# Optimization experiments

Measured on AMD Instinct MI355X. Metric: run time of the kernel, lower is better.

Reference implementation:

```python
import jax, jax.numpy as jnp
import numpy as np

SWITCH_W = 30.0
TOL = 5
DECAY = 0.7
FP_PEN = 10.0
INV_PEN = 100.0
CLASS_W = jnp.array([1.0, 1.0, SWITCH_W, SWITCH_W], dtype=jnp.float32)


def setup_inputs() -> dict:
    key = jax.random.key(0)
    k1, k2, k3 = jax.random.split(key, 3)
    B, S, C = 512, 8192, 4
    logits = jax.random.normal(k1, (B, S, C), dtype=jnp.float32)
    labels = jax.random.randint(k2, (B, S), 0, 4, dtype=jnp.int32)
    # sprinkle ignore_index (-100) positions like real padded sequences
    drop = jax.random.uniform(k3, (B, S)) < 0.05
    labels = jnp.where(drop, jnp.int32(-100), labels)
    return {"logits": logits, "labels": labels}


def _mode_multiplier(labels, preds):
    """Sequential state machine over time; carry = (pred_mode, true_mode) per batch row."""
    B, S = labels.shape

    def step(carry, xs):
        pm, tm = carry
        lab, pred = xs  # [B] each
        valid = lab != -100
        # invalid transition penalty on predicted switches
        bad = ((pred == 2) & (pm == 0)) | ((pred == 3) & (pm == 1))
        pen = jnp.where(valid & bad, INV_PEN, 1.0)
        new_pm = jnp.where(valid, jnp.where((pred == 0) | (pred == 2), 0, 1), pm)
        # reward correct mode switches (true label agrees with pred switch)
        good = ((lab == 2) & (tm == 1) & (pred == 2)) | ((lab == 3) & (tm == 0) & (pred == 3))
        bonus = jnp.where(valid & good, 0.1, 1.0)
        new_tm = jnp.where(valid & ((lab == 0) | (lab == 2)), 0,
                           jnp.where(valid & ((lab == 1) | (lab == 3)), 1, tm))
        return (new_pm, new_tm), pen * bonus

    init = (jnp.zeros((B,), jnp.int32), jnp.zeros((B,), jnp.int32))
    _, mult = jax.lax.scan(step, init, (labels.T, preds.T))
    return mult.T  # [B, S]


def _nearest_dist(mask):
    """For each position, distance to nearest True in the same row; BIG if none."""
    B, S = mask.shape
    BIG = jnp.int32(S + TOL + 2)

    def f(c, m):
        c = jnp.where(m, jnp.int32(0), jnp.minimum(c + 1, BIG))
        return c, c

    init = jnp.full((B,), BIG, jnp.int32)
    _, fwd = jax.lax.scan(f, init, mask.T)
    _, bwd = jax.lax.scan(f, init, mask[:, ::-1].T)
    return jnp.minimum(fwd.T, bwd.T[:, ::-1])


def _loss(logits, labels):
    preds = jnp.argmax(logits, axis=-1).astype(jnp.int32)
    valid = labels != -100
    labs = jnp.where(valid, labels, 0)
    logp = jax.nn.log_softmax(logits, axis=-1)
    ce = -jnp.take_along_axis(logp, labs[..., None], axis=-1)[..., 0] * CLASS_W[labs]

    mult = _mode_multiplier(labels, preds)
    for c in (2, 3):
        true_m = labels == c
        pred_m = preds == c
        d_true = _nearest_dist(true_m)
        d_pred = _nearest_dist(pred_m)
        has_true = true_m.any(axis=1, keepdims=True)
        has_pred = pred_m.any(axis=1, keepdims=True)
        # multipliers at predicted-switch positions
        mp = jnp.where(
            pred_m,
            jnp.where(
                has_true,
                jnp.where(d_true == 0, 0.1,
                          jnp.where(d_true <= TOL, DECAY ** d_true.astype(jnp.float32), FP_PEN)),
                FP_PEN * 2.0),
            1.0)
        # multipliers at true-switch positions
        mt = jnp.where(
            true_m,
            jnp.where(has_pred, jnp.where(d_pred > TOL, 2.0, 1.0), 3.0),
            1.0)
        mult = mult * mp * mt

    vf = valid.astype(ce.dtype)
    total = (ce * mult * vf).sum()
    return total / jnp.maximum(vf.sum(), 1.0)


def reference(logits, labels):
    return _loss(logits, labels)
```

## Files before the change

kernel.cpp:

```cpp
#include <hip/hip_runtime.h>
#include <math.h>

#define BROWS 512
#define SLEN  8192
#define NT    1024
#define CHUNK (SLEN / NT)
#define NWRD  (SLEN / 32)
#define MWRD  (NWRD + 2)

__device__ __forceinline__ int win_dist(const unsigned int* __restrict__ M, int t) {
    int sI = t + 27;
    int w  = sI >> 5;
    int off = sI & 31;
    unsigned long long val =
        ((unsigned long long)M[w] | ((unsigned long long)M[w + 1] << 32)) >> off;
    unsigned int win = (unsigned int)val & 0x7FFu;
    if (win & 32u) return 0;
    unsigned int dn = win & 31u;
    unsigned int up = (win >> 6) & 31u;
    int d = 99;
    if (dn) d = 5 - (31 - __clz((int)dn));
    if (up) { int du = __ffs((int)up); if (du < d) d = du; }
    return d;
}

__device__ __forceinline__ float decay_pow(int d) {
    return (d == 1) ? 0.7f : (d == 2) ? 0.49f : (d == 3) ? 0.343f
         : (d == 4) ? 0.2401f : 0.16807f;
}

__global__ __launch_bounds__(NT, 8) void row_loss_kernel(
    const float* __restrict__ logits, const int* __restrict__ labels,
    double* __restrict__ psum, unsigned int* __restrict__ pcnt)
{
    __shared__ float         s_ce[SLEN];
    __shared__ unsigned char s_pk[SLEN];
    __shared__ unsigned int  s_m[4][MWRD];
    __shared__ unsigned int  s_wave[16];
    __shared__ unsigned int  s_wavex[16];
    __shared__ unsigned int  s_flags;
    __shared__ double        s_red[16];
    __shared__ int           s_redc[16];

    const int row  = blockIdx.x;
    const int tid  = threadIdx.x;
    const int lane = tid & 63;
    const int wid  = tid >> 6;

    if (tid < 8) s_m[tid >> 1][(tid & 1) ? (MWRD - 1) : 0] = 0u;
    if (tid == 0) s_flags = 0u;

    const float4* lg4 = (const float4*)(logits + (size_t)row * SLEN * 4);
    const int*    lb  = labels + (size_t)row * SLEN;

    int cnt = 0;
    #pragma unroll
    for (int kk = 0; kk < CHUNK; kk += 4) {
        float4 v[4]; int la[4];
        #pragma unroll
        for (int j = 0; j < 4; ++j) {
            int t = (kk + j) * NT + tid;
            v[j]  = lg4[t];
            la[j] = lb[t];
        }
        #pragma unroll
        for (int j = 0; j < 4; ++j) {
            int t = (kk + j) * NT + tid;
            float4 q = v[j];
            int lab  = la[j];
            float m01 = fmaxf(q.x, q.y), m23 = fmaxf(q.z, q.w);
            float best = fmaxf(m01, m23);
            int pred = (best == q.x) ? 0 : (best == q.y) ? 1 : (best == q.z) ? 2 : 3;
            bool valid = (lab != -100);
            cnt += valid ? 1 : 0;
            int l = valid ? (lab & 3) : 0;
            float se = __expf(q.x - best) + __expf(q.y - best) +
                       __expf(q.z - best) + __expf(q.w - best);
            float lse = best + __logf(se);
            float xl = (l == 0) ? q.x : (l == 1) ? q.y : (l == 2) ? q.z : q.w;
            float wc = (l >= 2) ? 30.0f : 1.0f;
            s_ce[t] = valid ? (lse - xl) * wc : 0.0f;
            s_pk[t] = (unsigned char)(pred | (l << 2) | (valid ? 16 : 0));
        }
    }
    __syncthreads();

    const int base = tid * CHUNK;
    const unsigned long long pkw = *(const unsigned long long*)(s_pk + base);
    unsigned int mt2 = 0, mp2 = 0, mt3 = 0, mp3 = 0;
    unsigned int summary = 0;
    #pragma unroll
    for (int i = 0; i < CHUNK; ++i) {
        unsigned int pk = (unsigned int)(pkw >> (8 * i)) & 31u;
        int pred = pk & 3, l = (pk >> 2) & 3;
        bool valid = (pk & 16) != 0;
        if (pred == 2) mp2 |= 1u << i;
        if (pred == 3) mp3 |= 1u << i;
        if (valid && l == 2) mt2 |= 1u << i;
        if (valid && l == 3) mt3 |= 1u << i;
        if (valid) summary = 4u | (unsigned)(pred & 1) | ((unsigned)(l & 1) << 1);
    }
    {
        int sh = (tid & 3) * 8;
        unsigned int w0 = mt2 << sh, w1 = mp2 << sh, w2 = mt3 << sh, w3 = mp3 << sh;
        w0 |= __shfl_xor(w0, 1); w0 |= __shfl_xor(w0, 2);
        w1 |= __shfl_xor(w1, 1); w1 |= __shfl_xor(w1, 2);
        w2 |= __shfl_xor(w2, 1); w2 |= __shfl_xor(w2, 2);
        w3 |= __shfl_xor(w3, 1); w3 |= __shfl_xor(w3, 2);
        if ((tid & 3) == 0) {
            int wi = 1 + (tid >> 2);
            s_m[0][wi] = w0; s_m[1][wi] = w1; s_m[2][wi] = w2; s_m[3][wi] = w3;
        }
    }
    {
        unsigned int fl = (mt2 ? 1u : 0u) | (mp2 ? 2u : 0u) |
                          (mt3 ? 4u : 0u) | (mp3 ? 8u : 0u);
        #pragma unroll
        for (int s = 32; s > 0; s >>= 1) fl |= __shfl_xor(fl, s);
        if (lane == 0 && fl) atomicOr(&s_flags, fl);
    }

    unsigned int inc = summary;
    #pragma unroll
    for (int st = 1; st < 64; st <<= 1) {
        unsigned int o = __shfl_up(inc, st);
        if (lane >= st && !(inc & 4u)) inc = o;
    }
    unsigned int exc = __shfl_up(inc, 1);
    if (lane == 0) exc = 0u;
    if (lane == 63) s_wave[wid] = inc;
    __syncthreads();
    if (wid == 0) {
        unsigned int wv = (lane < 16) ? s_wave[lane] : 0u;
        #pragma unroll
        for (int st = 1; st < 16; st <<= 1) {
            unsigned int o = __shfl_up(wv, st);
            if (lane >= st && !(wv & 4u)) wv = o;
        }
        unsigned int wex = __shfl_up(wv, 1);
        if (lane == 0) wex = 0u;
        if (lane < 16) s_wavex[lane] = wex;
    }
    __syncthreads();

    unsigned int pre = (exc & 4u) ? exc : s_wavex[wid];
    int pm = (int)(pre & 1u), tm = (int)((pre >> 1) & 1u);
    const unsigned int flags = s_flags;
    const bool hasT2 = flags & 1u, hasP2 = flags & 2u;
    const bool hasT3 = flags & 4u, hasP3 = flags & 8u;

    float4 c0 = *(const float4*)(s_ce + base);
    float4 c1 = *(const float4*)(s_ce + base + 4);
    float cearr[8] = {c0.x, c0.y, c0.z, c0.w, c1.x, c1.y, c1.z, c1.w};

    float acc = 0.0f;
    #pragma unroll
    for (int i = 0; i < CHUNK; ++i) {
        int t = base + i;
        unsigned int pk = (unsigned int)(pkw >> (8 * i)) & 31u;
        int pred = pk & 3, l = (pk >> 2) & 3;
        bool valid = (pk & 16) != 0;
        float m = 1.0f;
        if (valid) {
            bool bad = (pred == 2 && pm == 0) || (pred == 3 && pm == 1);
            if (bad) m *= 100.0f;
            bool good = (l == 2 && tm == 1 && pred == 2) ||
                        (l == 3 && tm == 0 && pred == 3);
            if (good) m *= 0.1f;
            pm = pred & 1;
            tm = l & 1;
        }
        if (pred >= 2) {
            bool has = (pred == 2) ? hasT2 : hasT3;
            if (!has) m *= 20.0f;
            else {
                int d = win_dist(s_m[(pred - 2) << 1], t);
                m *= (d == 0) ? 0.1f : (d <= 5) ? decay_pow(d) : 10.0f;
            }
        }
        if (valid && l >= 2) {
            bool has = (l == 2) ? hasP2 : hasP3;
            if (!has) m *= 3.0f;
            else if (win_dist(s_m[1 + ((l - 2) << 1)], t) > 5) m *= 2.0f;
        }
        acc += cearr[i] * m;
    }

    double dacc = (double)acc;
    #pragma unroll
    for (int o = 32; o > 0; o >>= 1) {
        dacc += __shfl_down(dacc, o);
        cnt  += __shfl_down(cnt, o);
    }
    if (lane == 0) { s_red[wid] = dacc; s_redc[wid] = cnt; }
    __syncthreads();
    if (tid == 0) {
        double tot = 0.0; unsigned int c = 0;
        #pragma unroll
        for (int i = 0; i < 16; ++i) { tot += s_red[i]; c += (unsigned int)s_redc[i]; }
        psum[row] = tot;
        pcnt[row] = c;
    }
}

__global__ __launch_bounds__(512) void finalize_kernel(
    const double* __restrict__ psum, const unsigned int* __restrict__ pcnt,
    float* __restrict__ out)
{
    __shared__ double       sd[8];
    __shared__ unsigned int sc[8];
    int tid = threadIdx.x, lane = tid & 63, wid = tid >> 6;
    double v = psum[tid];
    unsigned int c = pcnt[tid];
    #pragma unroll
    for (int o = 32; o > 0; o >>= 1) {
        v += __shfl_down(v, o);
        c += __shfl_down(c, o);
    }
    if (lane == 0) { sd[wid] = v; sc[wid] = c; }
    __syncthreads();
    if (tid == 0) {
        double t = 0.0; unsigned int cc = 0;
        #pragma unroll
        for (int i = 0; i < 8; ++i) { t += sd[i]; cc += sc[i]; }
        double d = (cc > 0u) ? (double)cc : 1.0;
        out[0] = (float)(t / d);
    }
}

extern "C" void kernel_launch(void* const* d_in, const int* in_sizes, int n_in,
                              void* d_out, int out_size, void* d_ws, size_t ws_size,
                              hipStream_t stream) {
    const float* logits = (const float*)d_in[0];
    const int*   labels = (const int*)d_in[1];
    float* out = (float*)d_out;
    double* psum = (double*)d_ws;
    unsigned int* pcnt = (unsigned int*)(psum + BROWS);

    row_loss_kernel<<<BROWS, NT, 0, stream>>>(logits, labels, psum, pcnt);
    finalize_kernel<<<1, 512, 0, stream>>>(psum, pcnt, out);
}
```

Before: 113.0 us.

## Load contiguous per-thread chunks directly and drop shared-memory staging

Each thread now loads its own contiguous 8-element chunk of logits and labels from global memory, and keeps cross-entropy values and packed pred/label bits in registers. This removes the 40KB shared-memory staging arrays and a block barrier. The cross-wave prefix scan is now done redundantly by every wave instead of one wave plus a barrier. In exchange, the global loads are strided per thread rather than fully coalesced across a wavefront. Lower shared-memory use may also allow more blocks per CU.

```diff
diff --git a/kernel.cpp b/kernel.cpp
--- a/kernel.cpp
+++ b/kernel.cpp
@@ -4,7 +4,7 @@
 #define BROWS 512
 #define SLEN  8192
 #define NT    1024
-#define CHUNK (SLEN / NT)
+#define CHUNK 8
 #define NWRD  (SLEN / 32)
 #define MWRD  (NWRD + 2)
 
@@ -33,11 +33,8 @@
     const float* __restrict__ logits, const int* __restrict__ labels,
     double* __restrict__ psum, unsigned int* __restrict__ pcnt)
 {
-    __shared__ float         s_ce[SLEN];
-    __shared__ unsigned char s_pk[SLEN];
     __shared__ unsigned int  s_m[4][MWRD];
     __shared__ unsigned int  s_wave[16];
-    __shared__ unsigned int  s_wavex[16];
     __shared__ unsigned int  s_flags;
     __shared__ double        s_red[16];
     __shared__ int           s_redc[16];
@@ -46,60 +43,54 @@
     const int tid  = threadIdx.x;
     const int lane = tid & 63;
     const int wid  = tid >> 6;
-
-    if (tid < 8) s_m[tid >> 1][(tid & 1) ? (MWRD - 1) : 0] = 0u;
-    if (tid == 0) s_flags = 0u;
-
-    const float4* lg4 = (const float4*)(logits + (size_t)row * SLEN * 4);
-    const int*    lb  = labels + (size_t)row * SLEN;
-
+    const int base = tid * CHUNK;
+
+    if (tid < 4) { s_m[tid][0] = 0u; s_m[tid][MWRD - 1] = 0u; }
+    if (tid == 4) s_flags = 0u;
+
+    const float4* lg4 = (const float4*)logits + (size_t)row * SLEN + base;
+    const int4*   lb4 = (const int4*)(labels + (size_t)row * SLEN + base);
+
+    int4 la0 = lb4[0], la1 = lb4[1];
+    int labs[8] = {la0.x, la0.y, la0.z, la0.w, la1.x, la1.y, la1.z, la1.w};
+
+    float ce[8];
+    unsigned long long pkw = 0ull;
+    unsigned int mt2 = 0, mp2 = 0, mt3 = 0, mp3 = 0;
+    unsigned int summary = 0;
     int cnt = 0;
-    #pragma unroll
-    for (int kk = 0; kk < CHUNK; kk += 4) {
-        float4 v[4]; int la[4];
+
+    #pragma unroll
+    for (int b = 0; b < 2; ++b) {
+        float4 q[4];
+        #pragma unroll
+        for (int j = 0; j < 4; ++j) q[j] = lg4[b * 4 + j];
         #pragma unroll
         for (int j = 0; j < 4; ++j) {
-            int t = (kk + j) * NT + tid;
-            v[j]  = lg4[t];
-            la[j] = lb[t];
-        }
-        #pragma unroll
-        for (int j = 0; j < 4; ++j) {
-            int t = (kk + j) * NT + tid;
-            float4 q = v[j];
-            int lab  = la[j];
-            float m01 = fmaxf(q.x, q.y), m23 = fmaxf(q.z, q.w);
+            const int i = b * 4 + j;
+            float4 v = q[j];
+            int lab = labs[i];
+            float m01 = fmaxf(v.x, v.y), m23 = fmaxf(v.z, v.w);
             float best = fmaxf(m01, m23);
-            int pred = (best == q.x) ? 0 : (best == q.y) ? 1 : (best == q.z) ? 2 : 3;
+            int pred = (best == v.x) ? 0 : (best == v.y) ? 1 : (best == v.z) ? 2 : 3;
             bool valid = (lab != -100);
             cnt += valid ? 1 : 0;
             int l = valid ? (lab & 3) : 0;
-            float se = __expf(q.x - best) + __expf(q.y - best) +
-                       __expf(q.z - best) + __expf(q.w - best);
+            float se = __expf(v.x - best) + __expf(v.y - best) +
+                       __expf(v.z - best) + __expf(v.w - best);
             float lse = best + __logf(se);
-            float xl = (l == 0) ? q.x : (l == 1) ? q.y : (l == 2) ? q.z : q.w;
+            float xl = (l == 0) ? v.x : (l == 1) ? v.y : (l == 2) ? v.z : v.w;
             float wc = (l >= 2) ? 30.0f : 1.0f;
-            s_ce[t] = valid ? (lse - xl) * wc : 0.0f;
-            s_pk[t] = (unsigned char)(pred | (l << 2) | (valid ? 16 : 0));
-        }
-    }
-    __syncthreads();
-
-    const int base = tid * CHUNK;
-    const unsigned long long pkw = *(const unsigned long long*)(s_pk + base);
-    unsigned int mt2 = 0, mp2 = 0, mt3 = 0, mp3 = 0;
-    unsigned int summary = 0;
-    #pragma unroll
-    for (int i = 0; i < CHUNK; ++i) {
-        unsigned int pk = (unsigned int)(pkw >> (8 * i)) & 31u;
-        int pred = pk & 3, l = (pk >> 2) & 3;
-        bool valid = (pk & 16) != 0;
-        if (pred == 2) mp2 |= 1u << i;
-        if (pred == 3) mp3 |= 1u << i;
-        if (valid && l == 2) mt2 |= 1u << i;
-        if (valid && l == 3) mt3 |= 1u << i;
-        if (valid) summary = 4u | (unsigned)(pred & 1) | ((unsigned)(l & 1) << 1);
-    }
+            ce[i] = valid ? (lse - xl) * wc : 0.0f;
+            pkw |= (unsigned long long)(pred | (l << 2) | (valid ? 16 : 0)) << (8 * i);
+            if (pred == 2) mp2 |= 1u << i;
+            if (pred == 3) mp3 |= 1u << i;
+            if (valid && l == 2) mt2 |= 1u << i;
+            if (valid && l == 3) mt3 |= 1u << i;
+            if (valid) summary = 4u | (unsigned)(pred & 1) | ((unsigned)(l & 1) << 1);
+        }
+    }
+
     {
         int sh = (tid & 3) * 8;
         unsigned int w0 = mt2 << sh, w1 = mp2 << sh, w2 = mt3 << sh, w3 = mp3 << sh;
@@ -130,28 +121,21 @@
     if (lane == 0) exc = 0u;
     if (lane == 63) s_wave[wid] = inc;
     __syncthreads();
-    if (wid == 0) {
-        unsigned int wv = (lane < 16) ? s_wave[lane] : 0u;
-        #pragma unroll
-        for (int st = 1; st < 16; st <<= 1) {
-            unsigned int o = __shfl_up(wv, st);
-            if (lane >= st && !(wv & 4u)) wv = o;
-        }
-        unsigned int wex = __shfl_up(wv, 1);
-        if (lane == 0) wex = 0u;
-        if (lane < 16) s_wavex[lane] = wex;
-    }
-    __syncthreads();
-
-    unsigned int pre = (exc & 4u) ? exc : s_wavex[wid];
+
+    unsigned int wv = (lane < 16) ? s_wave[lane] : 0u;
+    #pragma unroll
+    for (int st = 1; st < 16; st <<= 1) {
+        unsigned int o = __shfl_up(wv, st);
+        if (lane >= st && !(wv & 4u)) wv = o;
+    }
+    unsigned int wpre = __shfl(wv, (wid > 0) ? (wid - 1) : 0);
+    if (wid == 0) wpre = 0u;
+
+    unsigned int pre = (exc & 4u) ? exc : wpre;
     int pm = (int)(pre & 1u), tm = (int)((pre >> 1) & 1u);
     const unsigned int flags = s_flags;
     const bool hasT2 = flags & 1u, hasP2 = flags & 2u;
     const bool hasT3 = flags & 4u, hasP3 = flags & 8u;
-
-    float4 c0 = *(const float4*)(s_ce + base);
-    float4 c1 = *(const float4*)(s_ce + base + 4);
-    float cearr[8] = {c0.x, c0.y, c0.z, c0.w, c1.x, c1.y, c1.z, c1.w};
 
     float acc = 0.0f;
     #pragma unroll
@@ -183,7 +167,7 @@
             if (!has) m *= 3.0f;
             else if (win_dist(s_m[1 + ((l - 2) << 1)], t) > 5) m *= 2.0f;
         }
-        acc += cearr[i] * m;
+        acc += ce[i] * m;
     }
 
     double dacc = (double)acc;
```

Measured after the change: 173.5 us. 53.5% more time.
